# Kernel tuning notes

Measured on AMD Instinct MI355X. Metric: run time of the kernel, lower is better.

## Reference

```python
import jax, jax.numpy as jnp
import numpy as np

BETA = 0.95
THRESHOLD = 1.0
ATAN_ALPHA = 2.0  # snntorch default ATan surrogate slope


@jax.custom_vjp
def spike_fn(u):
    # Heaviside spike with ATan surrogate gradient (snntorch default).
    return (u > 0).astype(u.dtype)

def _spike_fwd(u):
    return spike_fn(u), u

def _spike_bwd(u, g):
    grad = (ATAN_ALPHA / 2.0) / (1.0 + (jnp.pi / 2.0 * ATAN_ALPHA * u) ** 2)
    return (g * grad,)

spike_fn.defvjp(_spike_fwd, _spike_bwd)


def setup_inputs() -> dict:
    key = jax.random.key(0)
    k1, k2 = jax.random.split(key)
    x = jax.random.normal(k1, (255, 256, 784), dtype=jnp.float32)
    # Kaiming-ish init for Linear(784, 40, bias=False)
    W = jax.random.normal(k2, (40, 784), dtype=jnp.float32) * (1.0 / np.sqrt(784.0))
    return {"x": x, "W": W}


def reference(x, W):
    # x: [T, B, 784], W: [40, 784]
    B = x.shape[1]
    n_out = W.shape[0]
    mem0 = jnp.zeros((B, n_out), dtype=x.dtype)

    def step(mem, xt):
        cur = xt @ W.T                                  # [B, 40]
        reset = jax.lax.stop_gradient(
            (mem > THRESHOLD).astype(mem.dtype))        # detached, from prev mem
        mem_new = (BETA * mem + cur) * (1.0 - reset)    # zero-reset mechanism
        spk = spike_fn(mem_new - THRESHOLD)
        return mem_new, (spk, mem_new)

    _, (spk_rec, mem_rec) = jax.lax.scan(step, mem0, x)
    return spk_rec, mem_rec  # each [T, B, 40]
```

## Files before the change

### kernel.cpp

```cpp
#include <hip/hip_runtime.h>
#include <hip/hip_bf16.h>

#define T_STEPS 255
#define BATCH 256
#define NIN 784
#define NOUT 40
#define MROWS (T_STEPS * BATCH)
#define TBN (T_STEPS * BATCH * NOUT)
#define BN_CH (BATCH * NOUT)

#define BM 128
#define NCH 25
#define WB_CHUNK 4608
#define EPS_NEAR 2e-4f
#define SCH 30

typedef short bf16x8 __attribute__((ext_vector_type(8)));
typedef float f32x4 __attribute__((ext_vector_type(4)));

__device__ __forceinline__ unsigned short f2bf(float f) {
  unsigned u = __float_as_uint(f);
  u += 0x7fffu + ((u >> 16) & 1u);
  return (unsigned short)(u >> 16);
}
__device__ __forceinline__ float bf2f(unsigned short h) {
  return __uint_as_float(((unsigned)h) << 16);
}

__global__ __launch_bounds__(256) void wsplit_kernel(
    const float* __restrict__ W, unsigned short* __restrict__ Wbg,
    int* __restrict__ count) {
  int i = blockIdx.x * 256 + threadIdx.x;
  if (i == 0) *count = 0;
  if (i >= NCH * WB_CHUNK) return;
  int e = i & 7, l = (i >> 3) & 63, t = (i >> 9) % 3, s = (i / 1536) % 3,
      c = i / 4608;
  int k = c * 32 + (l >> 4) * 8 + e;
  int n = t * 16 + (l & 15);
  float v = (n < NOUT && k < NIN) ? W[n * NIN + k] : 0.f;
  unsigned short h1 = f2bf(v);
  float r1 = v - bf2f(h1);
  unsigned short h2 = f2bf(r1);
  float r2 = r1 - bf2f(h2);
  unsigned short h3 = f2bf(r2);
  Wbg[i] = (s == 0) ? h1 : (s == 1) ? h2 : h3;
}

__global__ __launch_bounds__(256) void lif_gemm_mfma(
    const float* __restrict__ X, const unsigned short* __restrict__ Wbg,
    float* __restrict__ cur) {
  alignas(16) __shared__ float xs[4096];
  const int tid = threadIdx.x;
  const int m0 = blockIdx.x * BM;
  const int w = tid >> 6, l = tid & 63;
  const int lr = l & 15, lg = l >> 4;

  f32x4 acc[2][3];
#pragma unroll
  for (int st = 0; st < 2; ++st)
#pragma unroll
    for (int t = 0; t < 3; ++t) acc[st][t] = (f32x4){0.f, 0.f, 0.f, 0.f};

  float4 gx[4];
  bf16x8 B[9], B2[9];

#define LOADX(C, DST)                                                     \
  do {                                                                    \
    const int k0_ = (C) * 32;                                             \
    _Pragma("unroll")                                                     \
    for (int i = 0; i < 4; ++i) {                                         \
      int S = tid + i * 256;                                              \
      int row = S >> 3;                                                   \
      int c4 = (S & 7) ^ (row & 7);                                       \
      int k = k0_ + c4 * 4;                                               \
      float4 v = make_float4(0.f, 0.f, 0.f, 0.f);                         \
      if (k < NIN)                                                        \
        v = *reinterpret_cast<const float4*>(X + (size_t)(m0 + row) * NIN + k); \
      DST[i] = v;                                                         \
    }                                                                     \
  } while (0)

#define LOADB(C, DST)                                                     \
  do {                                                                    \
    const unsigned short* base_ = Wbg + (size_t)(C) * WB_CHUNK;           \
    _Pragma("unroll")                                                     \
    for (int q = 0; q < 9; ++q)                                           \
      DST[q] = *reinterpret_cast<const bf16x8*>(base_ + (q * 64 + l) * 8); \
  } while (0)

#define WRITEX(SRC)                                                       \
  do {                                                                    \
    _Pragma("unroll")                                                     \
    for (int i = 0; i < 4; ++i) {                                         \
      int S = tid + i * 256;                                              \
      *reinterpret_cast<float4*>(&xs[S * 4]) = SRC[i];                    \
    }                                                                     \
  } while (0)

  LOADX(0, gx);
  LOADB(0, B);
  WRITEX(gx);
  __syncthreads();

  for (int c = 0; c < NCH; ++c) {
    const bool more = (c + 1 < NCH);
    if (more) {
      LOADX(c + 1, gx);
      LOADB(c + 1, B2);
    }

#pragma unroll
    for (int st = 0; st < 2; ++st) {
      int row = (w + st * 4) * 16 + lr;
      int sA = row * 8 + ((lg * 2) ^ (row & 7));
      int sB = row * 8 + ((lg * 2 + 1) ^ (row & 7));
      float4 fa = *reinterpret_cast<float4*>(&xs[sA * 4]);
      float4 fb = *reinterpret_cast<float4*>(&xs[sB * 4]);
      float f[8] = {fa.x, fa.y, fa.z, fa.w, fb.x, fb.y, fb.z, fb.w};
      union U { unsigned d[4]; bf16x8 v; } A1, A2, A3;
#pragma unroll
      for (int d = 0; d < 4; ++d) {
        float e0 = f[2 * d], e1 = f[2 * d + 1];
        unsigned short h0 = f2bf(e0), h1 = f2bf(e1);
        float r0 = e0 - bf2f(h0), r1 = e1 - bf2f(h1);
        unsigned short g0 = f2bf(r0), g1 = f2bf(r1);
        float s0 = r0 - bf2f(g0), s1 = r1 - bf2f(g1);
        A1.d[d] = (unsigned)h0 | ((unsigned)h1 << 16);
        A2.d[d] = (unsigned)g0 | ((unsigned)g1 << 16);
        A3.d[d] = (unsigned)f2bf(s0) | ((unsigned)f2bf(s1) << 16);
      }
#pragma unroll
      for (int t = 0; t < 3; ++t) {
        acc[st][t] = __builtin_amdgcn_mfma_f32_16x16x32_bf16(A3.v, B[0 * 3 + t], acc[st][t], 0, 0, 0);
        acc[st][t] = __builtin_amdgcn_mfma_f32_16x16x32_bf16(A1.v, B[2 * 3 + t], acc[st][t], 0, 0, 0);
        acc[st][t] = __builtin_amdgcn_mfma_f32_16x16x32_bf16(A2.v, B[1 * 3 + t], acc[st][t], 0, 0, 0);
        acc[st][t] = __builtin_amdgcn_mfma_f32_16x16x32_bf16(A2.v, B[0 * 3 + t], acc[st][t], 0, 0, 0);
        acc[st][t] = __builtin_amdgcn_mfma_f32_16x16x32_bf16(A1.v, B[1 * 3 + t], acc[st][t], 0, 0, 0);
        acc[st][t] = __builtin_amdgcn_mfma_f32_16x16x32_bf16(A1.v, B[0 * 3 + t], acc[st][t], 0, 0, 0);
      }
    }
    __syncthreads();
    if (more) {
      WRITEX(gx);
      __syncthreads();
#pragma unroll
      for (int q = 0; q < 9; ++q) B[q] = B2[q];
    }
  }
#undef LOADX
#undef LOADB
#undef WRITEX

#pragma unroll
  for (int st = 0; st < 2; ++st)
#pragma unroll
    for (int t = 0; t < 3; ++t)
#pragma unroll
      for (int r = 0; r < 4; ++r) {
        int col = t * 16 + lr;
        if (col < NOUT) {
          size_t grow = (size_t)m0 + (w + st * 4) * 16 + lg * 4 + r;
          cur[grow * NOUT + col] = acc[st][t][r];
        }
      }
}

__global__ __launch_bounds__(64) void lif_scan_kernel(
    float* __restrict__ spk, float* __restrict__ curmem,
    int* __restrict__ count, int* __restrict__ wlist) {
  const int idx = blockIdx.x * 64 + threadIdx.x;
  float mem = 0.f;
  bool near = false;
  float c[SCH];
#pragma unroll
  for (int i = 0; i < SCH; ++i) c[i] = curmem[(size_t)i * BN_CH + idx];
  for (int ch = 0; ch < 9; ++ch) {
    const int t0 = ch * SCH;
    float nx[SCH];
    if (ch != 8) {
#pragma unroll
      for (int i = 0; i < SCH; ++i) {
        int t = t0 + SCH + i;
        nx[i] = (t < T_STEPS) ? curmem[(size_t)t * BN_CH + idx] : 0.f;
      }
    }
#pragma unroll
    for (int i = 0; i < SCH; ++i) {
      if (t0 + i < T_STEPS) {
        float reset = (mem > 1.0f) ? 1.0f : 0.0f;
        float decay = 0.95f * mem;
        asm volatile("" : "+v"(decay));
        float summ = decay + c[i];
        float mnew = summ * (1.0f - reset);
        near = near || (fabsf(mnew - 1.0f) < EPS_NEAR);
        curmem[(size_t)(t0 + i) * BN_CH + idx] = mnew;
        spk[(size_t)(t0 + i) * BN_CH + idx] = (mnew > 1.0f) ? 1.0f : 0.0f;
        mem = mnew;
      }
    }
    if (ch != 8) {
#pragma unroll
      for (int i = 0; i < SCH; ++i) c[i] = nx[i];
    }
  }
  if (near) {
    int p = atomicAdd(count, 1);
    wlist[p] = idx;
  }
}

__global__ __launch_bounds__(256) void chaindot_kernel(
    const float* __restrict__ X, const float* __restrict__ W,
    const int* __restrict__ count, const int* __restrict__ wlist,
    float* __restrict__ curfix) {
  const int wv0 = blockIdx.x * 4 + (threadIdx.x >> 6);
  const int l = threadIdx.x & 63;
  const int njobs = *count * 32;
  for (int job = wv0; job < njobs; job += 10240) {
    const int f = job >> 5;
    const int tb = (job & 31) * 8;
    const int idx = wlist[f];
    const int b = idx / NOUT, n = idx % NOUT;
    double wreg[13];
#pragma unroll
    for (int j = 0; j < 12; ++j) wreg[j] = (double)W[n * NIN + l + j * 64];
    wreg[12] = (l < 16) ? (double)W[n * NIN + 768 + l] : 0.0;
#pragma unroll
    for (int u = 0; u < 8; ++u) {
      int t = tb + u;
      if (t >= T_STEPS) break;
      const float* xr = X + (size_t)(t * BATCH + b) * NIN;
      double s = 0.0;
#pragma unroll
      for (int j = 0; j < 12; ++j) s = fma((double)xr[l + j * 64], wreg[j], s);
      if (l < 16) s = fma((double)xr[768 + l], wreg[12], s);
#pragma unroll
      for (int off = 32; off; off >>= 1) s += __shfl_xor(s, off);
      if (l == 0) curfix[(size_t)f * T_STEPS + t] = (float)s;
    }
  }
}

__global__ __launch_bounds__(64) void chainscan_kernel(
    float* __restrict__ spk, float* __restrict__ memout,
    const int* __restrict__ count, const int* __restrict__ wlist,
    const float* __restrict__ curfix) {
  const int f = blockIdx.x * 64 + threadIdx.x;
  if (f >= *count) return;
  const int idx = wlist[f];
  const float* cf = curfix + (size_t)f * T_STEPS;
  float mem = 0.f;
  float c[15];
#pragma unroll
  for (int i = 0; i < 15; ++i) c[i] = cf[i];
  for (int ch = 0; ch < 17; ++ch) {
    const int t0 = ch * 15;
    float nx[15];
    if (ch != 16) {
#pragma unroll
      for (int i = 0; i < 15; ++i) nx[i] = cf[t0 + 15 + i];
    }
#pragma unroll
    for (int i = 0; i < 15; ++i) {
      float reset = (mem > 1.0f) ? 1.0f : 0.0f;
      float decay = 0.95f * mem;
      asm volatile("" : "+v"(decay));
      float summ = decay + c[i];
      float mnew = summ * (1.0f - reset);
      spk[(size_t)(t0 + i) * BN_CH + idx] = (mnew > 1.0f) ? 1.0f : 0.0f;
      memout[(size_t)(t0 + i) * BN_CH + idx] = mnew;
      mem = mnew;
    }
    if (ch != 16) {
#pragma unroll
      for (int i = 0; i < 15; ++i) c[i] = nx[i];
    }
  }
}

extern "C" void kernel_launch(void* const* d_in, const int* in_sizes, int n_in,
                              void* d_out, int out_size, void* d_ws,
                              size_t ws_size, hipStream_t stream) {
  (void)in_sizes; (void)n_in; (void)out_size; (void)ws_size;
  const float* X = (const float*)d_in[0];
  const float* W = (const float*)d_in[1];
  float* out = (float*)d_out;
  float* spk = out;
  float* memout = out + TBN;
  char* ws = (char*)d_ws;
  int* count = (int*)ws;
  int* wlist = (int*)(ws + 64);
  unsigned short* Wbg = (unsigned short*)(ws + 41024);
  float* curfix = (float*)(ws + 271424);

  wsplit_kernel<<<(NCH * WB_CHUNK + 255) / 256, 256, 0, stream>>>(W, Wbg,
                                                                  count);
  lif_gemm_mfma<<<MROWS / BM, 256, 0, stream>>>(X, Wbg, memout);
  lif_scan_kernel<<<BN_CH / 64, 64, 0, stream>>>(spk, memout, count, wlist);
  chaindot_kernel<<<2560, 256, 0, stream>>>(X, W, count, wlist, curfix);
  chainscan_kernel<<<BN_CH / 64, 64, 0, stream>>>(spk, memout, count, wlist,
                                                  curfix);
}
```

Measured before the change: 107.3 us.

## Double-buffer X tile in LDS to drop one barrier per K-chunk

Replaces the single shared-memory X tile with two ping-pong LDS buffers and manually unrolls the K loop by two. The write of the next chunk now overlaps compute on the current one, which removes one __syncthreads per chunk and drops the B-register copy. The cost is doubled LDS use (32 KB per block), which may lower occupancy, and extra register pressure from the two register sets.

```diff
diff --git a/kernel.cpp b/kernel.cpp
--- a/kernel.cpp
+++ b/kernel.cpp
@@ -49,7 +49,8 @@
 __global__ __launch_bounds__(256) void lif_gemm_mfma(
     const float* __restrict__ X, const unsigned short* __restrict__ Wbg,
     float* __restrict__ cur) {
-  alignas(16) __shared__ float xs[4096];
+  alignas(16) __shared__ float xs0[4096];
+  alignas(16) __shared__ float xs1[4096];
   const int tid = threadIdx.x;
   const int m0 = blockIdx.x * BM;
   const int w = tid >> 6, l = tid & 63;
@@ -61,8 +62,8 @@
 #pragma unroll
     for (int t = 0; t < 3; ++t) acc[st][t] = (f32x4){0.f, 0.f, 0.f, 0.f};
 
-  float4 gx[4];
-  bf16x8 B[9], B2[9];
+  float4 gxA[4], gxB[4];
+  bf16x8 BA[9], BB[9];
 
 #define LOADX(C, DST)                                                     \
   do {                                                                    \
@@ -88,68 +89,73 @@
       DST[q] = *reinterpret_cast<const bf16x8*>(base_ + (q * 64 + l) * 8); \
   } while (0)
 
-#define WRITEX(SRC)                                                       \
+#define WRITEX(BUF, SRC)                                                  \
   do {                                                                    \
     _Pragma("unroll")                                                     \
     for (int i = 0; i < 4; ++i) {                                         \
       int S = tid + i * 256;                                              \
-      *reinterpret_cast<float4*>(&xs[S * 4]) = SRC[i];                    \
+      *reinterpret_cast<float4*>(&(BUF)[S * 4]) = SRC[i];                 \
     }                                                                     \
   } while (0)
 
-  LOADX(0, gx);
-  LOADB(0, B);
-  WRITEX(gx);
+#define COMPUTE(BUF, BSET)                                                \
+  do {                                                                    \
+    _Pragma("unroll")                                                     \
+    for (int st = 0; st < 2; ++st) {                                      \
+      int row = (w + st * 4) * 16 + lr;                                   \
+      int sA = row * 8 + ((lg * 2) ^ (row & 7));                          \
+      int sB = row * 8 + ((lg * 2 + 1) ^ (row & 7));                      \
+      float4 fa = *reinterpret_cast<float4*>(&(BUF)[sA * 4]);             \
+      float4 fb = *reinterpret_cast<float4*>(&(BUF)[sB * 4]);             \
+      float f[8] = {fa.x, fa.y, fa.z, fa.w, fb.x, fb.y, fb.z, fb.w};      \
+      union U { unsigned d[4]; bf16x8 v; } A1, A2, A3;                    \
+      _Pragma("unroll")                                                   \
+      for (int d = 0; d < 4; ++d) {                                       \
+        float e0 = f[2 * d], e1 = f[2 * d + 1];                           \
+        unsigned short h0 = f2bf(e0), h1 = f2bf(e1);                      \
+        float r0 = e0 - bf2f(h0), r1 = e1 - bf2f(h1);                     \
+        unsigned short g0 = f2bf(r0), g1 = f2bf(r1);                      \
+        float s0 = r0 - bf2f(g0), s1 = r1 - bf2f(g1);                     \
+        A1.d[d] = (unsigned)h0 | ((unsigned)h1 << 16);                    \
+        A2.d[d] = (unsigned)g0 | ((unsigned)g1 << 16);                    \
+        A3.d[d] = (unsigned)f2bf(s0) | ((unsigned)f2bf(s1) << 16);        \
+      }                                                                   \
+      _Pragma("unroll")                                                   \
+      for (int t = 0; t < 3; ++t) {                                       \
+        acc[st][t] = __builtin_amdgcn_mfma_f32_16x16x32_bf16(A3.v, BSET[0 * 3 + t], acc[st][t], 0, 0, 0); \
+        acc[st][t] = __builtin_amdgcn_mfma_f32_16x16x32_bf16(A1.v, BSET[2 * 3 + t], acc[st][t], 0, 0, 0); \
+        acc[st][t] = __builtin_amdgcn_mfma_f32_16x16x32_bf16(A2.v, BSET[1 * 3 + t], acc[st][t], 0, 0, 0); \
+        acc[st][t] = __builtin_amdgcn_mfma_f32_16x16x32_bf16(A2.v, BSET[0 * 3 + t], acc[st][t], 0, 0, 0); \
+        acc[st][t] = __builtin_amdgcn_mfma_f32_16x16x32_bf16(A1.v, BSET[1 * 3 + t], acc[st][t], 0, 0, 0); \
+        acc[st][t] = __builtin_amdgcn_mfma_f32_16x16x32_bf16(A1.v, BSET[0 * 3 + t], acc[st][t], 0, 0, 0); \
+      }                                                                   \
+    }                                                                     \
+  } while (0)
+
+  LOADX(0, gxA);
+  LOADB(0, BA);
+  WRITEX(xs0, gxA);
+  LOADX(1, gxB);
+  LOADB(1, BB);
   __syncthreads();
 
-  for (int c = 0; c < NCH; ++c) {
-    const bool more = (c + 1 < NCH);
-    if (more) {
-      LOADX(c + 1, gx);
-      LOADB(c + 1, B2);
-    }
-
-#pragma unroll
-    for (int st = 0; st < 2; ++st) {
-      int row = (w + st * 4) * 16 + lr;
-      int sA = row * 8 + ((lg * 2) ^ (row & 7));
-      int sB = row * 8 + ((lg * 2 + 1) ^ (row & 7));
-      float4 fa = *reinterpret_cast<float4*>(&xs[sA * 4]);
-      float4 fb = *reinterpret_cast<float4*>(&xs[sB * 4]);
-      float f[8] = {fa.x, fa.y, fa.z, fa.w, fb.x, fb.y, fb.z, fb.w};
-      union U { unsigned d[4]; bf16x8 v; } A1, A2, A3;
-#pragma unroll
-      for (int d = 0; d < 4; ++d) {
-        float e0 = f[2 * d], e1 = f[2 * d + 1];
-        unsigned short h0 = f2bf(e0), h1 = f2bf(e1);
-        float r0 = e0 - bf2f(h0), r1 = e1 - bf2f(h1);
-        unsigned short g0 = f2bf(r0), g1 = f2bf(r1);
-        float s0 = r0 - bf2f(g0), s1 = r1 - bf2f(g1);
-        A1.d[d] = (unsigned)h0 | ((unsigned)h1 << 16);
-        A2.d[d] = (unsigned)g0 | ((unsigned)g1 << 16);
-        A3.d[d] = (unsigned)f2bf(s0) | ((unsigned)f2bf(s1) << 16);
-      }
-#pragma unroll
-      for (int t = 0; t < 3; ++t) {
-        acc[st][t] = __builtin_amdgcn_mfma_f32_16x16x32_bf16(A3.v, B[0 * 3 + t], acc[st][t], 0, 0, 0);
-        acc[st][t] = __builtin_amdgcn_mfma_f32_16x16x32_bf16(A1.v, B[2 * 3 + t], acc[st][t], 0, 0, 0);
-        acc[st][t] = __builtin_amdgcn_mfma_f32_16x16x32_bf16(A2.v, B[1 * 3 + t], acc[st][t], 0, 0, 0);
-        acc[st][t] = __builtin_amdgcn_mfma_f32_16x16x32_bf16(A2.v, B[0 * 3 + t], acc[st][t], 0, 0, 0);
-        acc[st][t] = __builtin_amdgcn_mfma_f32_16x16x32_bf16(A1.v, B[1 * 3 + t], acc[st][t], 0, 0, 0);
-        acc[st][t] = __builtin_amdgcn_mfma_f32_16x16x32_bf16(A1.v, B[0 * 3 + t], acc[st][t], 0, 0, 0);
-      }
-    }
+  for (int c = 0; c < 24; c += 2) {
+    WRITEX(xs1, gxB);
+    if (c + 2 < NCH) LOADX(c + 2, gxA);
+    COMPUTE(xs0, BA);
+    if (c + 2 < NCH) LOADB(c + 2, BA);
     __syncthreads();
-    if (more) {
-      WRITEX(gx);
-      __syncthreads();
-#pragma unroll
-      for (int q = 0; q < 9; ++q) B[q] = B2[q];
-    }
-  }
+    if (c + 2 < NCH) WRITEX(xs0, gxA);
+    if (c + 3 < NCH) LOADX(c + 3, gxB);
+    COMPUTE(xs1, BB);
+    if (c + 3 < NCH) LOADB(c + 3, BB);
+    __syncthreads();
+  }
+  COMPUTE(xs0, BA);
 #undef LOADX
 #undef LOADB
 #undef WRITEX
+#undef COMPUTE
 
 #pragma unroll
   for (int st = 0; st < 2; ++st)
```

Measured after the change: 107.1 us. Within noise of the previous version (-0.2%).
